# Optimization experiments

Measured on AMD Instinct MI355X. Metric: run time of the kernel, lower is better.

Reference implementation:

```python
import jax, jax.numpy as jnp
import numpy as np

BETA = 0.25
EPS_NORM = 1e-12

def _l2norm(x):
    # F.normalize(x, dim=-1): x / max(||x||, eps)
    n = jnp.sqrt(jnp.sum(x * x, axis=-1, keepdims=True))
    return x / jnp.maximum(n, EPS_NORM)

def setup_inputs() -> dict:
    key = jax.random.key(0)
    k1, k2 = jax.random.split(key)
    z = jax.random.normal(k1, (32, 4096, 256), dtype=jnp.float32)
    # matches nn.Embedding init uniform_(-1/num_embed, 1/num_embed)
    embed_weight = jax.random.uniform(k2, (1024, 256), dtype=jnp.float32,
                                      minval=-1.0 / 1024, maxval=1.0 / 1024)
    return {"z": z, "embed_weight": embed_weight}

def reference(z, embed_weight):
    num_embed, embed_dim = embed_weight.shape
    z_flat = z.reshape(-1, embed_dim)                      # [N, D]
    n_tok = z_flat.shape[0]

    # cosine distance: normalized z (detached) @ normalized codebook^T -> [N, K]
    zn = jax.lax.stop_gradient(_l2norm(z_flat))
    cn = _l2norm(embed_weight)
    d = zn @ cn.T                                          # [N, K]

    # torch sort(dim=1) then indices[:, -1] == argmax along codebook axis
    encoding_indices = jnp.argmax(d, axis=1)               # [N] int

    z_q = embed_weight[encoding_indices].reshape(z.shape)  # gather codebook rows

    # training losses (commitment + codebook)
    sg = jax.lax.stop_gradient
    loss = BETA * jnp.mean((sg(z_q) - z) ** 2) + jnp.mean((z_q - sg(z)) ** 2)

    # straight-through estimator
    z_q_st = z + sg(z_q - z)

    # perplexity from one-hot usage stats (counts instead of dense one-hot)
    counts = jnp.zeros((num_embed,), jnp.float32).at[encoding_indices].add(1.0)
    avg_probs = counts / jnp.float32(n_tok)
    perplexity = jnp.exp(-jnp.sum(avg_probs * jnp.log(avg_probs + 1e-10)))

    return z_q_st, loss, perplexity, encoding_indices
```

## Files before the change

kernel.cpp:

```cpp
#include <hip/hip_runtime.h>
#include <math.h>

#define N_TOK   131072
#define DIM     256
#define K_CODE  1024
#define KEXT    768
#define MARGIN  2e-3f

#define WS_COUNTS   0
#define WS_LOSS     4096
#define WS_RCOUNT   4104
#define WS_INVN     8192
#define WS_FIDX     16384
#define WS_RLIST    1048576
#define WS_BEXT     2097152

#define CHUNK_BYTES 49152

#define OUT_LOSS  33554432
#define OUT_PERP  33554433
#define OUT_IDX   33554434

typedef __bf16 bf16x8 __attribute__((ext_vector_type(8)));
typedef float  f32x4  __attribute__((ext_vector_type(4)));

static __device__ __forceinline__ unsigned short f2bf(float f) {
    unsigned int u = __float_as_uint(f);
    u += 0x7FFFu + ((u >> 16) & 1u);
    return (unsigned short)(u >> 16);
}
static __device__ __forceinline__ float bf2f(unsigned short h) {
    return __uint_as_float(((unsigned int)h) << 16);
}

static __device__ __forceinline__ void load_lds16(const void* g, void* l) {
    __builtin_amdgcn_global_load_lds(
        (const __attribute__((address_space(1))) unsigned int*)g,
        (__attribute__((address_space(3))) unsigned int*)l, 16, 0, 0);
}

__global__ void vq_norms(const float* __restrict__ embed, float* __restrict__ invn) {
    int lane = threadIdx.x & 63;
    int wave = (blockIdx.x * blockDim.x + threadIdx.x) >> 6;
    int nwav = (gridDim.x * blockDim.x) >> 6;
    for (int k = wave; k < K_CODE; k += nwav) {
        float4 v = *(const float4*)&embed[k * DIM + lane * 4];
        float s = v.x * v.x + v.y * v.y + v.z * v.z + v.w * v.w;
        #pragma unroll
        for (int off = 32; off; off >>= 1) s += __shfl_xor(s, off);
        if (lane == 0) invn[k] = 1.0f / fmaxf(sqrtf(s), 1e-12f);
    }
}

__global__ void vq_pack(const float* __restrict__ embed, unsigned short* __restrict__ bext) {
    int id = blockIdx.x * 256 + threadIdx.x;
    int k   = id / 96;
    int j8  = id - k * 96;
    int kk0 = j8 * 8;
    int src, hi;
    if (kk0 < 256)      { src = kk0;       hi = 1; }
    else if (kk0 < 512) { src = kk0 - 256; hi = 0; }
    else                { src = kk0 - 512; hi = 1; }
    const float* e = &embed[k * DIM + src];
    float4 f0 = *(const float4*)e;
    float4 f1 = *(const float4*)(e + 4);
    float v[8] = {f0.x, f0.y, f0.z, f0.w, f1.x, f1.y, f1.z, f1.w};
    unsigned short r[8] __attribute__((aligned(16)));
    #pragma unroll
    for (int j = 0; j < 8; ++j) {
        unsigned short h = f2bf(v[j]);
        r[j] = hi ? h : f2bf(v[j] - bf2f(h));
    }
    int c = k >> 5, kin = k & 31;
    int nt = kin >> 4, col = kin & 15;
    int ks = kk0 >> 5, quad = (kk0 >> 3) & 3;
    size_t dst = (size_t)c * CHUNK_BYTES + (size_t)(((nt * 24 + ks) * 64) + quad * 16 + col) * 16;
    *(float4*)((char*)bext + dst) = *(const float4*)r;
}

__launch_bounds__(256, 2)
__global__ void vq_argmax(const float* __restrict__ z,
                          const unsigned short* __restrict__ bext,
                          const float* __restrict__ invn, int* __restrict__ fidx,
                          int* __restrict__ rcount, int* __restrict__ rlist) {
    __shared__ unsigned short bbuf[CHUNK_BYTES / 2];

    const int tid  = threadIdx.x;
    const int w    = tid >> 6;
    const int lane = tid & 63;
    const int col  = lane & 15;
    const int quad = lane >> 4;
    const int tokBase = blockIdx.x * 128;

    bf16x8 ah[2][8], al[2][8];
    #pragma unroll
    for (int mt = 0; mt < 2; ++mt) {
        const float* zr = z + (size_t)(tokBase + w * 32 + mt * 16 + col) * DIM;
        #pragma unroll
        for (int ks = 0; ks < 8; ++ks) {
            float4 f0 = *(const float4*)(zr + ks * 32 + quad * 8);
            float4 f1 = *(const float4*)(zr + ks * 32 + quad * 8 + 4);
            float v[8] = {f0.x, f0.y, f0.z, f0.w, f1.x, f1.y, f1.z, f1.w};
            union { bf16x8 v; unsigned short u[8]; } th, tl;
            #pragma unroll
            for (int j = 0; j < 8; ++j) {
                unsigned short h = f2bf(v[j]);
                th.u[j] = h;
                tl.u[j] = f2bf(v[j] - bf2f(h));
            }
            ah[mt][ks] = th.v;
            al[mt][ks] = tl.v;
        }
    }

    float best[2][4], second[2][4];
    int   bidx[2][4];
    #pragma unroll
    for (int mt = 0; mt < 2; ++mt)
        #pragma unroll
        for (int r = 0; r < 4; ++r) { best[mt][r] = -1e30f; second[mt][r] = -1e30f; bidx[mt][r] = 0; }

    for (int c = 0; c < 32; ++c) {
        __syncthreads();
        {
            const char* gsrc = (const char*)bext + (size_t)c * CHUNK_BYTES;
            #pragma unroll
            for (int i = 0; i < 12; ++i) {
                int seg = w * 12 + i;
                load_lds16(gsrc + (size_t)seg * 1024 + lane * 16,
                           (char*)bbuf + seg * 1024);
            }
        }
        __syncthreads();

        f32x4 acc[2][2];
        #pragma unroll
        for (int mt = 0; mt < 2; ++mt)
            #pragma unroll
            for (int nt = 0; nt < 2; ++nt) acc[mt][nt] = (f32x4){0.f, 0.f, 0.f, 0.f};

        #pragma unroll
        for (int nt = 0; nt < 2; ++nt) {
            const unsigned short* bb = bbuf + nt * 24 * 512;
            #pragma unroll
            for (int ks = 0; ks < 8; ++ks) {
                bf16x8 b = *(const bf16x8*)&bb[ks * 512 + lane * 8];
                acc[0][nt] = __builtin_amdgcn_mfma_f32_16x16x32_bf16(ah[0][ks], b, acc[0][nt], 0, 0, 0);
                acc[1][nt] = __builtin_amdgcn_mfma_f32_16x16x32_bf16(ah[1][ks], b, acc[1][nt], 0, 0, 0);
            }
            #pragma unroll
            for (int ks = 0; ks < 8; ++ks) {
                bf16x8 b = *(const bf16x8*)&bb[(8 + ks) * 512 + lane * 8];
                acc[0][nt] = __builtin_amdgcn_mfma_f32_16x16x32_bf16(ah[0][ks], b, acc[0][nt], 0, 0, 0);
                acc[1][nt] = __builtin_amdgcn_mfma_f32_16x16x32_bf16(ah[1][ks], b, acc[1][nt], 0, 0, 0);
            }
            #pragma unroll
            for (int ks = 0; ks < 8; ++ks) {
                bf16x8 b = *(const bf16x8*)&bb[(16 + ks) * 512 + lane * 8];
                acc[0][nt] = __builtin_amdgcn_mfma_f32_16x16x32_bf16(al[0][ks], b, acc[0][nt], 0, 0, 0);
                acc[1][nt] = __builtin_amdgcn_mfma_f32_16x16x32_bf16(al[1][ks], b, acc[1][nt], 0, 0, 0);
            }
        }

        #pragma unroll
        for (int nt = 0; nt < 2; ++nt) {
            int code = c * 32 + nt * 16 + col;
            float iv = invn[code];
            #pragma unroll
            for (int mt = 0; mt < 2; ++mt)
                #pragma unroll
                for (int r = 0; r < 4; ++r) {
                    float v = acc[mt][nt][r] * iv;
                    if (v > best[mt][r]) { second[mt][r] = best[mt][r]; best[mt][r] = v; bidx[mt][r] = code; }
                    else                 { second[mt][r] = fmaxf(second[mt][r], v); }
                }
        }
    }

    #pragma unroll
    for (int mt = 0; mt < 2; ++mt)
        #pragma unroll
        for (int r = 0; r < 4; ++r) {
            float B = best[mt][r], S = second[mt][r];
            int   I = bidx[mt][r];
            #pragma unroll
            for (int off = 1; off < 16; off <<= 1) {
                float ob = __shfl_xor(B, off);
                float os = __shfl_xor(S, off);
                int   oi = __shfl_xor(I, off);
                if (ob > B) {
                    S = fmaxf(B, os);
                    B = ob; I = oi;
                } else {
                    if (ob == B && oi < I) I = oi;
                    S = fmaxf(S, ob);
                }
            }
            if (col == 0) {
                int token = tokBase + w * 32 + mt * 16 + quad * 4 + r;
                fidx[token] = I;
                if (B - S < MARGIN) {
                    int p = atomicAdd(rcount, 1);
                    rlist[p] = token;
                }
            }
        }
}

__global__ void vq_recheck(const float* __restrict__ z, const float* __restrict__ embed,
                           const int* __restrict__ rcount, const int* __restrict__ rlist,
                           int* __restrict__ fidx) {
    __shared__ double zd[DIM];
    __shared__ double rv[256];
    __shared__ int    rix[256];
    const int cnt = *rcount;
    for (int li = blockIdx.x; li < cnt; li += gridDim.x) {
        int token = rlist[li];
        __syncthreads();
        zd[threadIdx.x] = (double)z[token * DIM + threadIdx.x];
        __syncthreads();
        double bv = -1e300;
        int    bi = 0;
        #pragma unroll
        for (int j = 0; j < 4; ++j) {
            int k = threadIdx.x * 4 + j;
            const float* e = &embed[k * DIM];
            double acc = 0.0, nrm = 0.0;
            for (int d = 0; d < DIM; d += 4) {
                float4 ef = *(const float4*)&e[d];
                acc += (double)ef.x * zd[d]     + (double)ef.y * zd[d + 1] +
                       (double)ef.z * zd[d + 2] + (double)ef.w * zd[d + 3];
                nrm += (double)ef.x * ef.x + (double)ef.y * ef.y +
                       (double)ef.z * ef.z + (double)ef.w * ef.w;
            }
            double val = acc / fmax(sqrt(nrm), 1e-12);
            if (val > bv) { bv = val; bi = k; }
        }
        rv[threadIdx.x]  = bv;
        rix[threadIdx.x] = bi;
        __syncthreads();
        for (int s = 128; s; s >>= 1) {
            if (threadIdx.x < s) {
                double v2 = rv[threadIdx.x + s];
                int    i2 = rix[threadIdx.x + s];
                if (v2 > rv[threadIdx.x] ||
                    (v2 == rv[threadIdx.x] && i2 < rix[threadIdx.x])) {
                    rv[threadIdx.x] = v2;
                    rix[threadIdx.x] = i2;
                }
            }
            __syncthreads();
        }
        if (threadIdx.x == 0) fidx[token] = rix[0];
    }
}

__global__ void vq_output(const float* __restrict__ z, const float* __restrict__ embed,
                          const int* __restrict__ fidx, float* __restrict__ out,
                          int* __restrict__ counts, double* __restrict__ lossAcc) {
    int lane = threadIdx.x & 63;
    int gw   = (blockIdx.x * blockDim.x + threadIdx.x) >> 6;
    int nwav = (gridDim.x * blockDim.x) >> 6;
    double lsum = 0.0;
    for (int t = gw; t < N_TOK; t += nwav) {
        int idx = fidx[t];
        float4 e  = *(const float4*)&embed[idx * DIM + lane * 4];
        float4 zz = *(const float4*)&z[(size_t)t * DIM + lane * 4];
        float4 r, o;
        r.x = e.x - zz.x; r.y = e.y - zz.y; r.z = e.z - zz.z; r.w = e.w - zz.w;
        o.x = zz.x + r.x; o.y = zz.y + r.y; o.z = zz.z + r.z; o.w = zz.w + r.w;
        *(float4*)&out[(size_t)t * DIM + lane * 4] = o;
        lsum += (double)r.x * r.x + (double)r.y * r.y +
                (double)r.z * r.z + (double)r.w * r.w;
        if (lane == 0) {
            atomicAdd(&counts[idx], 1);
            out[OUT_IDX + t] = (float)idx;
        }
    }
    #pragma unroll
    for (int off = 32; off; off >>= 1) lsum += __shfl_down(lsum, off);
    if (lane == 0) atomicAdd(lossAcc, lsum);
}

__global__ void vq_finalize(const int* __restrict__ counts,
                            const double* __restrict__ lossAcc,
                            float* __restrict__ out) {
    __shared__ double sh[256];
    double s = 0.0;
    for (int b = threadIdx.x; b < K_CODE; b += 256) {
        double p = (double)counts[b] / (double)N_TOK;
        s += p * log(p + 1e-10);
    }
    sh[threadIdx.x] = s;
    __syncthreads();
    for (int st = 128; st; st >>= 1) {
        if (threadIdx.x < st) sh[threadIdx.x] += sh[threadIdx.x + st];
        __syncthreads();
    }
    if (threadIdx.x == 0) {
        out[OUT_PERP] = (float)exp(-sh[0]);
        out[OUT_LOSS] = (float)(1.25 * (*lossAcc) / (double)(N_TOK) / (double)(DIM));
    }
}

extern "C" void kernel_launch(void* const* d_in, const int* in_sizes, int n_in,
                              void* d_out, int out_size, void* d_ws, size_t ws_size,
                              hipStream_t stream) {
    const float* z     = (const float*)d_in[0];
    const float* embed = (const float*)d_in[1];
    float* out = (float*)d_out;
    char*  ws  = (char*)d_ws;

    int*            counts  = (int*)   (ws + WS_COUNTS);
    double*         lossAcc = (double*)(ws + WS_LOSS);
    int*            rcount  = (int*)   (ws + WS_RCOUNT);
    float*          invn    = (float*) (ws + WS_INVN);
    int*            fidx    = (int*)   (ws + WS_FIDX);
    int*            rlist   = (int*)   (ws + WS_RLIST);
    unsigned short* bext    = (unsigned short*)(ws + WS_BEXT);

    hipMemsetAsync(ws, 0, 16384, stream);

    vq_norms  <<<16,   256, 0, stream>>>(embed, invn);
    vq_pack   <<<384,  256, 0, stream>>>(embed, bext);
    vq_argmax <<<N_TOK / 128, 256, 0, stream>>>(z, bext, invn, fidx, rcount, rlist);
    vq_recheck<<<512,  256, 0, stream>>>(z, embed, rcount, rlist, fidx);
    vq_output <<<2048, 256, 0, stream>>>(z, embed, fidx, out, counts, lossAcc);
    vq_finalize<<<1,   256, 0, stream>>>(counts, lossAcc, out);
}
```

Before: 642.9 us.

## Double-buffer codebook chunks in LDS with 512-thread blocks and cached norms

The argmax kernel now uses 512-thread blocks covering 256 tokens each, with two LDS buffers so the next codebook chunk streams in while MFMA compute runs on the current one. Explicit vmcnt waits and raw barriers replace the two syncthreads per chunk. Inverse codebook norms are cached in shared memory, and the MFMA section runs at raised wave priority. LDS use roughly doubles, which with 512 threads per block may limit occupancy, and the hand-tuned waitcnt and barrier sequencing is fragile.

```diff
diff --git a/kernel.cpp b/kernel.cpp
--- a/kernel.cpp
+++ b/kernel.cpp
@@ -78,19 +78,25 @@
     *(float4*)((char*)bext + dst) = *(const float4*)r;
 }
 
-__launch_bounds__(256, 2)
+__launch_bounds__(512, 2)
 __global__ void vq_argmax(const float* __restrict__ z,
                           const unsigned short* __restrict__ bext,
                           const float* __restrict__ invn, int* __restrict__ fidx,
                           int* __restrict__ rcount, int* __restrict__ rlist) {
-    __shared__ unsigned short bbuf[CHUNK_BYTES / 2];
+    __shared__ unsigned short b0[CHUNK_BYTES / 2];
+    __shared__ unsigned short b1[CHUNK_BYTES / 2];
+    __shared__ float invn_s[K_CODE];
 
     const int tid  = threadIdx.x;
     const int w    = tid >> 6;
     const int lane = tid & 63;
     const int col  = lane & 15;
     const int quad = lane >> 4;
-    const int tokBase = blockIdx.x * 128;
+    const int tokBase = blockIdx.x * 256;
+
+    invn_s[tid]       = invn[tid];
+    invn_s[tid + 512] = invn[tid + 512];
+    asm volatile("s_waitcnt lgkmcnt(0)" ::: "memory");
 
     bf16x8 ah[2][8], al[2][8];
     #pragma unroll
@@ -113,6 +119,16 @@
         }
     }
 
+    auto stage = [&](int c, unsigned short* buf) {
+        const char* gsrc = (const char*)bext + (size_t)c * CHUNK_BYTES;
+        #pragma unroll
+        for (int i = 0; i < 6; ++i) {
+            int seg = w * 6 + i;
+            load_lds16(gsrc + (size_t)seg * 1024 + lane * 16,
+                       (char*)buf + seg * 1024);
+        }
+    };
+
     float best[2][4], second[2][4];
     int   bidx[2][4];
     #pragma unroll
@@ -120,25 +136,14 @@
         #pragma unroll
         for (int r = 0; r < 4; ++r) { best[mt][r] = -1e30f; second[mt][r] = -1e30f; bidx[mt][r] = 0; }
 
-    for (int c = 0; c < 32; ++c) {
-        __syncthreads();
-        {
-            const char* gsrc = (const char*)bext + (size_t)c * CHUNK_BYTES;
-            #pragma unroll
-            for (int i = 0; i < 12; ++i) {
-                int seg = w * 12 + i;
-                load_lds16(gsrc + (size_t)seg * 1024 + lane * 16,
-                           (char*)bbuf + seg * 1024);
-            }
-        }
-        __syncthreads();
-
+    auto compute = [&](int c, const unsigned short* bbuf) {
         f32x4 acc[2][2];
         #pragma unroll
         for (int mt = 0; mt < 2; ++mt)
             #pragma unroll
             for (int nt = 0; nt < 2; ++nt) acc[mt][nt] = (f32x4){0.f, 0.f, 0.f, 0.f};
 
+        __builtin_amdgcn_s_setprio(1);
         #pragma unroll
         for (int nt = 0; nt < 2; ++nt) {
             const unsigned short* bb = bbuf + nt * 24 * 512;
@@ -161,11 +166,12 @@
                 acc[1][nt] = __builtin_amdgcn_mfma_f32_16x16x32_bf16(al[1][ks], b, acc[1][nt], 0, 0, 0);
             }
         }
+        __builtin_amdgcn_s_setprio(0);
 
         #pragma unroll
         for (int nt = 0; nt < 2; ++nt) {
             int code = c * 32 + nt * 16 + col;
-            float iv = invn[code];
+            float iv = invn_s[code];
             #pragma unroll
             for (int mt = 0; mt < 2; ++mt)
                 #pragma unroll
@@ -175,6 +181,30 @@
                     else                 { second[mt][r] = fmaxf(second[mt][r], v); }
                 }
         }
+    };
+
+    __builtin_amdgcn_sched_barrier(0);
+    stage(0, b0);
+    stage(1, b1);
+
+    #pragma unroll 1
+    for (int cc = 0; cc < 32; cc += 2) {
+        asm volatile("s_waitcnt vmcnt(6)" ::: "memory");
+        __builtin_amdgcn_s_barrier();
+        __builtin_amdgcn_sched_barrier(0);
+        compute(cc, b0);
+        __builtin_amdgcn_sched_barrier(0);
+        __builtin_amdgcn_s_barrier();
+        if (cc + 2 < 32) stage(cc + 2, b0);
+
+        if (cc == 30) { asm volatile("s_waitcnt vmcnt(0)" ::: "memory"); }
+        else          { asm volatile("s_waitcnt vmcnt(6)" ::: "memory"); }
+        __builtin_amdgcn_s_barrier();
+        __builtin_amdgcn_sched_barrier(0);
+        compute(cc + 1, b1);
+        __builtin_amdgcn_sched_barrier(0);
+        __builtin_amdgcn_s_barrier();
+        if (cc + 3 < 32) stage(cc + 3, b1);
     }
 
     #pragma unroll
@@ -323,7 +353,7 @@
 
     vq_norms  <<<16,   256, 0, stream>>>(embed, invn);
     vq_pack   <<<384,  256, 0, stream>>>(embed, bext);
-    vq_argmax <<<N_TOK / 128, 256, 0, stream>>>(z, bext, invn, fidx, rcount, rlist);
+    vq_argmax <<<N_TOK / 256, 512, 0, stream>>>(z, bext, invn, fidx, rcount, rlist);
     vq_recheck<<<512,  256, 0, stream>>>(z, embed, rcount, rlist, fidx);
     vq_output <<<2048, 256, 0, stream>>>(z, embed, fidx, out, counts, lossAcc);
     vq_finalize<<<1,   256, 0, stream>>>(counts, lossAcc, out);
```

Measured after the change: 642.4 us. No clear change (-0.1%).

## Fold norms into pack, drop memset, fuse finalize via last-block pattern

Applied to the files above, without the earlier changes.

Codebook norms are now computed inside the pack kernel and applied before the bf16 hi/lo split, so the argmax kernel no longer multiplies by per-code inverse norms. Block 0 of the pack kernel zeros the workspace header instead of a separate memset. The finalize kernel is merged into the output kernel with an atomic done-counter, so the last block computes perplexity and loss. This removes three launches and a little per-element work, at the cost of a threadfence and atomic per block and a change in rounding, since normalized values are now what get split into bf16.

```diff
diff --git a/kernel.cpp b/kernel.cpp
--- a/kernel.cpp
+++ b/kernel.cpp
@@ -10,7 +10,7 @@
 #define WS_COUNTS   0
 #define WS_LOSS     4096
 #define WS_RCOUNT   4104
-#define WS_INVN     8192
+#define WS_DONE     4112
 #define WS_FIDX     16384
 #define WS_RLIST    1048576
 #define WS_BEXT     2097152
@@ -39,49 +39,59 @@
         (__attribute__((address_space(3))) unsigned int*)l, 16, 0, 0);
 }
 
-__global__ void vq_norms(const float* __restrict__ embed, float* __restrict__ invn) {
-    int lane = threadIdx.x & 63;
-    int wave = (blockIdx.x * blockDim.x + threadIdx.x) >> 6;
-    int nwav = (gridDim.x * blockDim.x) >> 6;
-    for (int k = wave; k < K_CODE; k += nwav) {
+__global__ void vq_pack(const float* __restrict__ embed, unsigned short* __restrict__ bext,
+                        int* __restrict__ wshdr) {
+    __shared__ float cs[4][DIM];
+    const int tid  = threadIdx.x;
+    const int w    = tid >> 6;
+    const int lane = tid & 63;
+    const int k0   = blockIdx.x * 4;
+
+    if (blockIdx.x == 0) {
+        for (int i = tid; i < 4096; i += 256) wshdr[i] = 0;
+    }
+
+    {
+        const int k = k0 + w;
         float4 v = *(const float4*)&embed[k * DIM + lane * 4];
         float s = v.x * v.x + v.y * v.y + v.z * v.z + v.w * v.w;
         #pragma unroll
         for (int off = 32; off; off >>= 1) s += __shfl_xor(s, off);
-        if (lane == 0) invn[k] = 1.0f / fmaxf(sqrtf(s), 1e-12f);
-    }
-}
-
-__global__ void vq_pack(const float* __restrict__ embed, unsigned short* __restrict__ bext) {
-    int id = blockIdx.x * 256 + threadIdx.x;
-    int k   = id / 96;
-    int j8  = id - k * 96;
-    int kk0 = j8 * 8;
-    int src, hi;
-    if (kk0 < 256)      { src = kk0;       hi = 1; }
-    else if (kk0 < 512) { src = kk0 - 256; hi = 0; }
-    else                { src = kk0 - 512; hi = 1; }
-    const float* e = &embed[k * DIM + src];
-    float4 f0 = *(const float4*)e;
-    float4 f1 = *(const float4*)(e + 4);
-    float v[8] = {f0.x, f0.y, f0.z, f0.w, f1.x, f1.y, f1.z, f1.w};
-    unsigned short r[8] __attribute__((aligned(16)));
-    #pragma unroll
-    for (int j = 0; j < 8; ++j) {
-        unsigned short h = f2bf(v[j]);
-        r[j] = hi ? h : f2bf(v[j] - bf2f(h));
-    }
-    int c = k >> 5, kin = k & 31;
-    int nt = kin >> 4, col = kin & 15;
-    int ks = kk0 >> 5, quad = (kk0 >> 3) & 3;
-    size_t dst = (size_t)c * CHUNK_BYTES + (size_t)(((nt * 24 + ks) * 64) + quad * 16 + col) * 16;
-    *(float4*)((char*)bext + dst) = *(const float4*)r;
+        float inv = 1.0f / fmaxf(sqrtf(s), 1e-12f);
+        float4 nv;
+        nv.x = v.x * inv; nv.y = v.y * inv; nv.z = v.z * inv; nv.w = v.w * inv;
+        *(float4*)&cs[w][lane * 4] = nv;
+    }
+    __syncthreads();
+
+    for (int t = tid; t < 384; t += 256) {
+        int lc  = t / 96;
+        int g   = t - lc * 96;
+        int k   = k0 + lc;
+        int kk0 = g * 8;
+        int src, hi;
+        if (kk0 < 256)      { src = kk0;       hi = 1; }
+        else if (kk0 < 512) { src = kk0 - 256; hi = 0; }
+        else                { src = kk0 - 512; hi = 1; }
+        unsigned short r[8] __attribute__((aligned(16)));
+        #pragma unroll
+        for (int j = 0; j < 8; ++j) {
+            float vv = cs[lc][src + j];
+            unsigned short h = f2bf(vv);
+            r[j] = hi ? h : f2bf(vv - bf2f(h));
+        }
+        int c = k >> 5, kin = k & 31;
+        int nt = kin >> 4, col = kin & 15;
+        int ks = kk0 >> 5, quad = (kk0 >> 3) & 3;
+        size_t dst = (size_t)c * CHUNK_BYTES + (size_t)(((nt * 24 + ks) * 64) + quad * 16 + col) * 16;
+        *(float4*)((char*)bext + dst) = *(const float4*)r;
+    }
 }
 
 __launch_bounds__(256, 2)
 __global__ void vq_argmax(const float* __restrict__ z,
                           const unsigned short* __restrict__ bext,
-                          const float* __restrict__ invn, int* __restrict__ fidx,
+                          int* __restrict__ fidx,
                           int* __restrict__ rcount, int* __restrict__ rlist) {
     __shared__ unsigned short bbuf[CHUNK_BYTES / 2];
 
@@ -165,12 +175,11 @@
         #pragma unroll
         for (int nt = 0; nt < 2; ++nt) {
             int code = c * 32 + nt * 16 + col;
-            float iv = invn[code];
             #pragma unroll
             for (int mt = 0; mt < 2; ++mt)
                 #pragma unroll
                 for (int r = 0; r < 4; ++r) {
-                    float v = acc[mt][nt][r] * iv;
+                    float v = acc[mt][nt][r];
                     if (v > best[mt][r]) { second[mt][r] = best[mt][r]; best[mt][r] = v; bidx[mt][r] = code; }
                     else                 { second[mt][r] = fmaxf(second[mt][r], v); }
                 }
@@ -257,7 +266,10 @@
 
 __global__ void vq_output(const float* __restrict__ z, const float* __restrict__ embed,
                           const int* __restrict__ fidx, float* __restrict__ out,
-                          int* __restrict__ counts, double* __restrict__ lossAcc) {
+                          int* __restrict__ counts, double* __restrict__ lossAcc,
+                          int* __restrict__ done) {
+    __shared__ double sh[256];
+    __shared__ int lastFlag;
     int lane = threadIdx.x & 63;
     int gw   = (blockIdx.x * blockDim.x + threadIdx.x) >> 6;
     int nwav = (gridDim.x * blockDim.x) >> 6;
@@ -280,26 +292,31 @@
     #pragma unroll
     for (int off = 32; off; off >>= 1) lsum += __shfl_down(lsum, off);
     if (lane == 0) atomicAdd(lossAcc, lsum);
-}
-
-__global__ void vq_finalize(const int* __restrict__ counts,
-                            const double* __restrict__ lossAcc,
-                            float* __restrict__ out) {
-    __shared__ double sh[256];
-    double s = 0.0;
-    for (int b = threadIdx.x; b < K_CODE; b += 256) {
-        double p = (double)counts[b] / (double)N_TOK;
-        s += p * log(p + 1e-10);
-    }
-    sh[threadIdx.x] = s;
+
+    __threadfence();
     __syncthreads();
-    for (int st = 128; st; st >>= 1) {
-        if (threadIdx.x < st) sh[threadIdx.x] += sh[threadIdx.x + st];
-        __syncthreads();
-    }
     if (threadIdx.x == 0) {
-        out[OUT_PERP] = (float)exp(-sh[0]);
-        out[OUT_LOSS] = (float)(1.25 * (*lossAcc) / (double)(N_TOK) / (double)(DIM));
+        int p = atomicAdd(done, 1);
+        lastFlag = (p == (int)gridDim.x - 1);
+    }
+    __syncthreads();
+    if (lastFlag) {
+        __threadfence();
+        double s = 0.0;
+        for (int b = threadIdx.x; b < K_CODE; b += 256) {
+            double p = (double)counts[b] / (double)N_TOK;
+            s += p * log(p + 1e-10);
+        }
+        sh[threadIdx.x] = s;
+        __syncthreads();
+        for (int st = 128; st; st >>= 1) {
+            if (threadIdx.x < st) sh[threadIdx.x] += sh[threadIdx.x + st];
+            __syncthreads();
+        }
+        if (threadIdx.x == 0) {
+            out[OUT_PERP] = (float)exp(-sh[0]);
+            out[OUT_LOSS] = (float)(1.25 * (*lossAcc) / (double)(N_TOK) / (double)(DIM));
+        }
     }
 }
 
@@ -314,17 +331,13 @@
     int*            counts  = (int*)   (ws + WS_COUNTS);
     double*         lossAcc = (double*)(ws + WS_LOSS);
     int*            rcount  = (int*)   (ws + WS_RCOUNT);
-    float*          invn    = (float*) (ws + WS_INVN);
+    int*            done    = (int*)   (ws + WS_DONE);
     int*            fidx    = (int*)   (ws + WS_FIDX);
     int*            rlist   = (int*)   (ws + WS_RLIST);
     unsigned short* bext    = (unsigned short*)(ws + WS_BEXT);
 
-    hipMemsetAsync(ws, 0, 16384, stream);
-
-    vq_norms  <<<16,   256, 0, stream>>>(embed, invn);
-    vq_pack   <<<384,  256, 0, stream>>>(embed, bext);
-    vq_argmax <<<N_TOK / 128, 256, 0, stream>>>(z, bext, invn, fidx, rcount, rlist);
+    vq_pack   <<<256,  256, 0, stream>>>(embed, bext, (int*)ws);
+    vq_argmax <<<N_TOK / 128, 256, 0, stream>>>(z, bext, fidx, rcount, rlist);
     vq_recheck<<<512,  256, 0, stream>>>(z, embed, rcount, rlist, fidx);
-    vq_output <<<2048, 256, 0, stream>>>(z, embed, fidx, out, counts, lossAcc);
-    vq_finalize<<<1,   256, 0, stream>>>(counts, lossAcc, out);
-}
+    vq_output <<<2048, 256, 0, stream>>>(z, embed, fidx, out, counts, lossAcc, done);
+}
```

Result: slower. 787.3 us (+22.5%).
